# Kernel tuning notes

Measured on AMD Instinct MI355X. Metric: run time of the kernel, lower is better.

The kernel has to match this reference:

```python
import jax, jax.numpy as jnp
import numpy as np

N_NODES = 100000
N_EDGES = 1600000
D = 64


def setup_inputs() -> dict:
    key = jax.random.key(0)
    ks = jax.random.split(key, 8)
    x = jax.random.normal(ks[0], (N_NODES, D), dtype=jnp.float32)
    edge_index = jax.random.randint(ks[1], (2, N_EDGES), 0, N_NODES, dtype=jnp.int64)
    scale = 1.0 / np.sqrt(D)
    W1 = jax.random.normal(ks[2], (D, D), dtype=jnp.float32) * scale
    W2 = jax.random.normal(ks[3], (D, D), dtype=jnp.float32) * scale
    W3 = jax.random.normal(ks[4], (D, D), dtype=jnp.float32) * scale
    b1 = jnp.zeros((D,), dtype=jnp.float32)
    b2 = jnp.zeros((D,), dtype=jnp.float32)
    b3 = jnp.zeros((D,), dtype=jnp.float32)
    return {"x": x, "edge_index": edge_index, "W1": W1, "b1": b1,
            "W2": W2, "b2": b2, "W3": W3, "b3": b3}


def reference(x, edge_index, W1, b1, W2, b2, W3, b3):
    # 3-layer GCN (PyG GCNConv semantics): add self-loops, symmetric
    # degree normalization, linear transform, scatter-add aggregation.
    # Dropout is identity at inference.
    N = x.shape[0]
    loops = jnp.arange(N, dtype=edge_index.dtype)
    src = jnp.concatenate([edge_index[0], loops])  # [E+N]
    dst = jnp.concatenate([edge_index[1], loops])  # [E+N]
    # degree of each node (in-degree at dst, self-loops included)
    deg = jax.ops.segment_sum(jnp.ones(src.shape[0], dtype=x.dtype), dst,
                              num_segments=N)
    dis = jnp.where(deg > 0, jax.lax.rsqrt(jnp.maximum(deg, 1.0)), 0.0)
    norm = dis[src] * dis[dst]  # [E+N]

    def gcn_layer(h, W, b):
        h = h @ W                                   # [N, d_out]
        msg = norm[:, None] * h[src]                # gather + scale, [E+N, d_out]
        agg = jax.ops.segment_sum(msg, dst, num_segments=N)  # scatter-add
        return agg + b

    h = jax.nn.relu(gcn_layer(x, W1, b1))
    h = jax.nn.relu(gcn_layer(h, W2, b2))
    return gcn_layer(h, W3, b3)
```

## Files before the change

### kernel.cpp

```cpp
#include <hip/hip_runtime.h>

#define NN 100000
#define NE 1600000

typedef __attribute__((ext_vector_type(16))) int i32x16;

#define NBKT 391
#define NBLK 256
#define EPB  (NE / NBLK)
#define PTH  512
#define TOT  (NBKT * NBLK)
#define SB   ((TOT + 1023) / 1024)

__global__ __launch_bounds__(PTH) void k_pcount(const int* __restrict__ dst,
                                                int* __restrict__ pcount) {
  __shared__ int lcnt[NBKT];
  int t = threadIdx.x, b = blockIdx.x;
  for (int i = t; i < NBKT; i += PTH) lcnt[i] = 0;
  __syncthreads();
  int base = b * EPB;
  for (int i = t; i < EPB; i += PTH)
    atomicAdd(&lcnt[dst[base + i] >> 8], 1);
  __syncthreads();
  for (int i = t; i < NBKT; i += PTH)
    pcount[i * NBLK + b] = lcnt[i];
}

__global__ __launch_bounds__(256) void k_pscan1(int* __restrict__ pcount,
                                                int* __restrict__ bsum) {
  __shared__ int sh[256];
  int t = threadIdx.x, b = blockIdx.x;
  int base = b * 1024 + t * 4;
  int v0 = (base + 0 < TOT) ? pcount[base + 0] : 0;
  int v1 = (base + 1 < TOT) ? pcount[base + 1] : 0;
  int v2 = (base + 2 < TOT) ? pcount[base + 2] : 0;
  int v3 = (base + 3 < TOT) ? pcount[base + 3] : 0;
  int s = v0 + v1 + v2 + v3;
  sh[t] = s;
  __syncthreads();
  for (int off = 1; off < 256; off <<= 1) {
    int x = (t >= off) ? sh[t - off] : 0;
    __syncthreads();
    sh[t] += x;
    __syncthreads();
  }
  int ex = sh[t] - s;
  if (t == 255) bsum[b] = sh[255];
  if (base + 0 < TOT) pcount[base + 0] = ex; ex += v0;
  if (base + 1 < TOT) pcount[base + 1] = ex; ex += v1;
  if (base + 2 < TOT) pcount[base + 2] = ex; ex += v2;
  if (base + 3 < TOT) pcount[base + 3] = ex;
}

__global__ __launch_bounds__(128) void k_pscan2(int* __restrict__ bsum) {
  __shared__ int sh[128];
  int t = threadIdx.x;
  int v = (t < SB) ? bsum[t] : 0;
  sh[t] = v;
  __syncthreads();
  for (int off = 1; off < 128; off <<= 1) {
    int x = (t >= off) ? sh[t - off] : 0;
    __syncthreads();
    sh[t] += x;
    __syncthreads();
  }
  if (t < SB) bsum[t] = sh[t] - v;
}

__global__ __launch_bounds__(256) void k_pscan3(int* __restrict__ pcount,
                                                const int* __restrict__ bsum) {
  int t = threadIdx.x, b = blockIdx.x;
  int add = bsum[b];
  int base = b * 1024 + t * 4;
  #pragma unroll
  for (int k = 0; k < 4; ++k)
    if (base + k < TOT) pcount[base + k] += add;
}

__global__ __launch_bounds__(PTH) void k_pscatter(const int* __restrict__ src,
                                                  const int* __restrict__ dst,
                                                  const int* __restrict__ pcount,
                                                  int* __restrict__ staged) {
  __shared__ int lpos[NBKT];
  int t = threadIdx.x, b = blockIdx.x;
  for (int i = t; i < NBKT; i += PTH) lpos[i] = pcount[i * NBLK + b];
  __syncthreads();
  int base = b * EPB;
  for (int i = t; i < EPB; i += PTH) {
    int s = src[base + i], d = dst[base + i];
    int pos = atomicAdd(&lpos[d >> 8], 1);
    staged[pos] = s | ((d & 255) << 17);
  }
}

__global__ __launch_bounds__(PTH) void k_bucket(const int* __restrict__ staged,
                                                const int* __restrict__ pcount,
                                                int* __restrict__ rowptr,
                                                float* __restrict__ dis,
                                                int* __restrict__ col) {
  __shared__ int lcnt[256];
  __shared__ int lscan[PTH];
  __shared__ int lpos[256];
  int t = threadIdx.x, bkt = blockIdx.x;
  int sbeg = pcount[bkt * NBLK];
  int send = (bkt == NBKT - 1) ? NE : pcount[(bkt + 1) * NBLK];

  if (t < 256) lcnt[t] = 0;
  __syncthreads();
  for (int i = sbeg + t; i < send; i += PTH)
    atomicAdd(&lcnt[(unsigned)staged[i] >> 17], 1);
  __syncthreads();

  int v = (t < 256) ? lcnt[t] : 0;
  lscan[t] = v;
  __syncthreads();
  for (int off = 1; off < PTH; off <<= 1) {
    int x = (t >= off) ? lscan[t - off] : 0;
    __syncthreads();
    lscan[t] += x;
    __syncthreads();
  }
  if (t < 256) {
    int gbase = sbeg + lscan[t] - v;
    int node = bkt * 256 + t;
    if (node < NN) {
      rowptr[node] = gbase;
      dis[node] = rsqrtf((float)(v + 1));
    }
    lpos[t] = gbase;
    if (bkt == NBKT - 1 && t == 0) rowptr[NN] = NE;
  }
  __syncthreads();

  for (int i = sbeg + t; i < send; i += PTH) {
    int e = staged[i];
    col[atomicAdd(&lpos[(unsigned)e >> 17], 1)] = e & 0x1FFFF;
  }
}

__device__ __forceinline__ unsigned bf16rne(float x) {
  unsigned u = __float_as_uint(x);
  return (u + 0x7fffu + ((u >> 16) & 1u)) >> 16;
}

__global__ __launch_bounds__(256) void k_xform(const float* __restrict__ h,
                                               const float* __restrict__ W,
                                               const float* __restrict__ dis,
                                               unsigned short* __restrict__ ts) {
  __shared__ float hT[64][132];
  __shared__ float Wl[64][68];
  const int tid = threadIdx.x;
  const int R0 = blockIdx.x * 128;

  {
    const float4* W4 = (const float4*)W;
    #pragma unroll
    for (int j = 0; j < 4; ++j) {
      int idx = tid + 256 * j;
      float4 v = W4[idx];
      int k = idx >> 4;
      int c = (idx & 15) * 4;
      Wl[k][c + 0] = v.x; Wl[k][c + 1] = v.y;
      Wl[k][c + 2] = v.z; Wl[k][c + 3] = v.w;
    }
  }
  {
    #pragma unroll
    for (int j = 0; j < 8; ++j) {
      int idx = tid + 256 * j;
      int r = idx >> 4;
      int k = (idx & 15) * 4;
      int rg = R0 + r; if (rg > NN - 1) rg = NN - 1;
      float4 v = *(const float4*)(h + (size_t)rg * 64 + k);
      hT[k + 0][r] = v.x; hT[k + 1][r] = v.y;
      hT[k + 2][r] = v.z; hT[k + 3][r] = v.w;
    }
  }
  __syncthreads();

  const int tx = tid & 7;
  const int ty = tid >> 3;
  float acc[4][8];
  #pragma unroll
  for (int i = 0; i < 4; ++i)
    #pragma unroll
    for (int j = 0; j < 8; ++j) acc[i][j] = 0.f;

  #pragma unroll 4
  for (int k = 0; k < 64; ++k) {
    float4 hv = *(const float4*)&hT[k][ty * 4];
    float4 w0 = *(const float4*)&Wl[k][tx * 8];
    float4 w1 = *(const float4*)&Wl[k][tx * 8 + 4];
    float hh[4] = {hv.x, hv.y, hv.z, hv.w};
    float wc[8] = {w0.x, w0.y, w0.z, w0.w, w1.x, w1.y, w1.z, w1.w};
    #pragma unroll
    for (int i = 0; i < 4; ++i)
      #pragma unroll
      for (int j = 0; j < 8; ++j)
        acc[i][j] = fmaf(hh[i], wc[j], acc[i][j]);
  }

  #pragma unroll
  for (int i = 0; i < 4; ++i) {
    int r = R0 + ty * 4 + i;
    if (r < NN) {
      float dr = dis[r];
      uint4 pk;
      pk.x = bf16rne(acc[i][0] * dr) | (bf16rne(acc[i][1] * dr) << 16);
      pk.y = bf16rne(acc[i][2] * dr) | (bf16rne(acc[i][3] * dr) << 16);
      pk.z = bf16rne(acc[i][4] * dr) | (bf16rne(acc[i][5] * dr) << 16);
      pk.w = bf16rne(acc[i][6] * dr) | (bf16rne(acc[i][7] * dr) << 16);
      *(uint4*)(ts + (size_t)r * 64 + tx * 8) = pk;
    }
  }
}

__global__ __launch_bounds__(256) void k_fuse(
    const unsigned short* __restrict__ ts, const int* __restrict__ rowptr,
    const int* __restrict__ col, const float* __restrict__ dis,
    const float* __restrict__ bias, const float* __restrict__ Wn,
    unsigned short* __restrict__ tnext)
{
  __shared__ float Wl[64][68];
  __shared__ float hh[32][68];
  const int tid  = threadIdx.x;
  const int lane = tid & 63;
  const int slot = lane >> 4;
  const int fq   = lane & 15;
  const int R0   = blockIdx.x * 32;
  const int wloc = tid >> 6;
  const int wid  = __builtin_amdgcn_readfirstlane(
                     (int)(blockIdx.x * 4 + wloc));
  const int n0   = wid * 8;

  {
    const float4* W4 = (const float4*)Wn;
    #pragma unroll
    for (int j = 0; j < 4; ++j) {
      int idx = tid + 256 * j;
      float4 v = W4[idx];
      int k = idx >> 4;
      int c = (idx & 15) * 4;
      Wl[k][c + 0] = v.x; Wl[k][c + 1] = v.y;
      Wl[k][c + 2] = v.z; Wl[k][c + 3] = v.w;
    }
  }

  const float4 bv = *(const float4*)(bias + fq * 4);
  const float m_self = (slot == 0) ? 1.f : 0.f;

  i32x16 rp;
  asm volatile("s_load_dwordx16 %0, %1, 0x0\n\ts_waitcnt lgkmcnt(0)"
               : "=s"(rp) : "s"(rowptr + n0));

  float a[8][4];
  #pragma unroll
  for (int i = 0; i < 8; ++i) {
    const uint2 sv = *(const uint2*)(ts + (size_t)(n0 + i) * 64 + fq * 4);
    a[i][0] = m_self * __uint_as_float(sv.x << 16);
    a[i][1] = m_self * __uint_as_float(sv.x & 0xffff0000u);
    a[i][2] = m_self * __uint_as_float(sv.y << 16);
    a[i][3] = m_self * __uint_as_float(sv.y & 0xffff0000u);
  }

  #pragma unroll
  for (int i = 0; i < 8; ++i) {
    const int r0 = rp[i], r1 = rp[i + 1];
    #pragma unroll
    for (int s = 0; s < 4; ++s) {
      int e = r0 + s * 4 + slot;
      int c = col[e];
      bool valid = e < r1;
      c = valid ? c : 0;
      float m = valid ? 1.f : 0.f;
      const uint2 gv = *(const uint2*)(ts + (size_t)c * 64 + fq * 4);
      a[i][0] = fmaf(m, __uint_as_float(gv.x << 16),         a[i][0]);
      a[i][1] = fmaf(m, __uint_as_float(gv.x & 0xffff0000u), a[i][1]);
      a[i][2] = fmaf(m, __uint_as_float(gv.y << 16),         a[i][2]);
      a[i][3] = fmaf(m, __uint_as_float(gv.y & 0xffff0000u), a[i][3]);
    }
  }

  #pragma unroll
  for (int i = 0; i < 8; ++i) {
    const int r1 = rp[i + 1];
    #pragma unroll 1
    for (int e0 = rp[i] + 16; e0 < r1; e0 += 8) {
      #pragma unroll
      for (int s = 0; s < 2; ++s) {
        int e = e0 + s * 4 + slot;
        int c = col[e];
        bool valid = e < r1;
        c = valid ? c : 0;
        float m = valid ? 1.f : 0.f;
        const uint2 gv = *(const uint2*)(ts + (size_t)c * 64 + fq * 4);
        a[i][0] = fmaf(m, __uint_as_float(gv.x << 16),         a[i][0]);
        a[i][1] = fmaf(m, __uint_as_float(gv.x & 0xffff0000u), a[i][1]);
        a[i][2] = fmaf(m, __uint_as_float(gv.y << 16),         a[i][2]);
        a[i][3] = fmaf(m, __uint_as_float(gv.y & 0xffff0000u), a[i][3]);
      }
    }
  }

  #pragma unroll
  for (int i = 0; i < 8; ++i) {
    const int node = n0 + i;
    const float dn = dis[node];
    float s0 = a[i][0], s1 = a[i][1], s2 = a[i][2], s3 = a[i][3];
    s0 += __shfl_xor(s0, 16); s1 += __shfl_xor(s1, 16);
    s2 += __shfl_xor(s2, 16); s3 += __shfl_xor(s3, 16);
    s0 += __shfl_xor(s0, 32); s1 += __shfl_xor(s1, 32);
    s2 += __shfl_xor(s2, 32); s3 += __shfl_xor(s3, 32);
    float4 o;
    o.x = fmaxf(fmaf(dn, s0, bv.x), 0.f);
    o.y = fmaxf(fmaf(dn, s1, bv.y), 0.f);
    o.z = fmaxf(fmaf(dn, s2, bv.z), 0.f);
    o.w = fmaxf(fmaf(dn, s3, bv.w), 0.f);
    if (lane < 16)
      *(float4*)&hh[wloc * 8 + i][fq * 4] = o;
  }
  __syncthreads();

  const int tx = tid & 7;
  const int ty = tid >> 3;
  float acc[8];
  #pragma unroll
  for (int j = 0; j < 8; ++j) acc[j] = 0.f;
  #pragma unroll 4
  for (int k = 0; k < 64; ++k) {
    float hkv = hh[ty][k];
    float4 w0 = *(const float4*)&Wl[k][tx * 8];
    float4 w1 = *(const float4*)&Wl[k][tx * 8 + 4];
    acc[0] = fmaf(hkv, w0.x, acc[0]); acc[1] = fmaf(hkv, w0.y, acc[1]);
    acc[2] = fmaf(hkv, w0.z, acc[2]); acc[3] = fmaf(hkv, w0.w, acc[3]);
    acc[4] = fmaf(hkv, w1.x, acc[4]); acc[5] = fmaf(hkv, w1.y, acc[5]);
    acc[6] = fmaf(hkv, w1.z, acc[6]); acc[7] = fmaf(hkv, w1.w, acc[7]);
  }
  {
    int r = R0 + ty;
    float dr = dis[r];
    uint4 pk;
    pk.x = bf16rne(acc[0] * dr) | (bf16rne(acc[1] * dr) << 16);
    pk.y = bf16rne(acc[2] * dr) | (bf16rne(acc[3] * dr) << 16);
    pk.z = bf16rne(acc[4] * dr) | (bf16rne(acc[5] * dr) << 16);
    pk.w = bf16rne(acc[6] * dr) | (bf16rne(acc[7] * dr) << 16);
    *(uint4*)(tnext + (size_t)r * 64 + tx * 8) = pk;
  }
}

__global__ __launch_bounds__(256) void k_agg(
    const unsigned short* __restrict__ ts, const int* __restrict__ rowptr,
    const int* __restrict__ col, const float* __restrict__ dis,
    const float* __restrict__ bias, float* __restrict__ out)
{
  const int lane = threadIdx.x & 63;
  const int slot = lane >> 4;
  const int fq   = lane & 15;
  const int wid  = __builtin_amdgcn_readfirstlane(
                     (int)((blockIdx.x * blockDim.x + threadIdx.x) >> 6));
  const int n0   = wid * 8;
  if (n0 >= NN) return;

  const float4 bv = *(const float4*)(bias + fq * 4);
  const float m_self = (slot == 0) ? 1.f : 0.f;

  i32x16 rp;
  asm volatile("s_load_dwordx16 %0, %1, 0x0\n\ts_waitcnt lgkmcnt(0)"
               : "=s"(rp) : "s"(rowptr + n0));

  float a[8][4];
  #pragma unroll
  for (int i = 0; i < 8; ++i) {
    const uint2 sv = *(const uint2*)(ts + (size_t)(n0 + i) * 64 + fq * 4);
    a[i][0] = m_self * __uint_as_float(sv.x << 16);
    a[i][1] = m_self * __uint_as_float(sv.x & 0xffff0000u);
    a[i][2] = m_self * __uint_as_float(sv.y << 16);
    a[i][3] = m_self * __uint_as_float(sv.y & 0xffff0000u);
  }

  #pragma unroll
  for (int i = 0; i < 8; ++i) {
    const int r0 = rp[i], r1 = rp[i + 1];
    #pragma unroll
    for (int s = 0; s < 4; ++s) {
      int e = r0 + s * 4 + slot;
      int c = col[e];
      bool valid = e < r1;
      c = valid ? c : 0;
      float m = valid ? 1.f : 0.f;
      const uint2 gv = *(const uint2*)(ts + (size_t)c * 64 + fq * 4);
      a[i][0] = fmaf(m, __uint_as_float(gv.x << 16),         a[i][0]);
      a[i][1] = fmaf(m, __uint_as_float(gv.x & 0xffff0000u), a[i][1]);
      a[i][2] = fmaf(m, __uint_as_float(gv.y << 16),         a[i][2]);
      a[i][3] = fmaf(m, __uint_as_float(gv.y & 0xffff0000u), a[i][3]);
    }
  }

  #pragma unroll
  for (int i = 0; i < 8; ++i) {
    const int r1 = rp[i + 1];
    #pragma unroll 1
    for (int e0 = rp[i] + 16; e0 < r1; e0 += 8) {
      #pragma unroll
      for (int s = 0; s < 2; ++s) {
        int e = e0 + s * 4 + slot;
        int c = col[e];
        bool valid = e < r1;
        c = valid ? c : 0;
        float m = valid ? 1.f : 0.f;
        const uint2 gv = *(const uint2*)(ts + (size_t)c * 64 + fq * 4);
        a[i][0] = fmaf(m, __uint_as_float(gv.x << 16),         a[i][0]);
        a[i][1] = fmaf(m, __uint_as_float(gv.x & 0xffff0000u), a[i][1]);
        a[i][2] = fmaf(m, __uint_as_float(gv.y << 16),         a[i][2]);
        a[i][3] = fmaf(m, __uint_as_float(gv.y & 0xffff0000u), a[i][3]);
      }
    }
  }

  #pragma unroll
  for (int i = 0; i < 8; ++i) {
    const int node = n0 + i;
    const float dn = dis[node];
    float s0 = a[i][0], s1 = a[i][1], s2 = a[i][2], s3 = a[i][3];
    s0 += __shfl_xor(s0, 16); s1 += __shfl_xor(s1, 16);
    s2 += __shfl_xor(s2, 16); s3 += __shfl_xor(s3, 16);
    s0 += __shfl_xor(s0, 32); s1 += __shfl_xor(s1, 32);
    s2 += __shfl_xor(s2, 32); s3 += __shfl_xor(s3, 32);
    float4 o;
    o.x = fmaf(dn, s0, bv.x); o.y = fmaf(dn, s1, bv.y);
    o.z = fmaf(dn, s2, bv.z); o.w = fmaf(dn, s3, bv.w);
    if (lane < 16)
      *(float4*)(out + (size_t)node * 64 + fq * 4) = o;
  }
}

extern "C" void kernel_launch(void* const* d_in, const int* in_sizes, int n_in,
                              void* d_out, int out_size, void* d_ws, size_t ws_size,
                              hipStream_t stream) {
  const float* x  = (const float*)d_in[0];
  const int*   ei = (const int*)d_in[1];
  const float* W1 = (const float*)d_in[2];
  const float* b1 = (const float*)d_in[3];
  const float* W2 = (const float*)d_in[4];
  const float* b2 = (const float*)d_in[5];
  const float* W3 = (const float*)d_in[6];
  const float* b3 = (const float*)d_in[7];
  float* out = (float*)d_out;

  const int* src = ei;
  const int* dst = ei + NE;

  char* ws = (char*)d_ws;
  size_t off = 0;
  auto alloc = [&](size_t bytes) {
    void* p = ws + off;
    off = (off + bytes + 255) & ~(size_t)255;
    return p;
  };
  int*   pcount = (int*)alloc((size_t)TOT * 4);
  int*   bsum   = (int*)alloc((size_t)SB * 4);
  int*   rowptr = (int*)alloc((size_t)(NN + 1 + 16) * 4);
  float* dis    = (float*)alloc((size_t)NN * 4);
  int*   staged = (int*)alloc((size_t)NE * 4);
  int*   col    = (int*)alloc((size_t)(NE + 64) * 4);
  unsigned short* tb1 =
      (unsigned short*)alloc((size_t)NN * 64 * 2);
  unsigned short* tb2 =
      (unsigned short*)alloc((size_t)NN * 64 * 2);
  (void)ws_size; (void)in_sizes; (void)n_in; (void)out_size;

  k_pcount  <<<NBLK, PTH, 0, stream>>>(dst, pcount);
  k_pscan1  <<<SB, 256, 0, stream>>>(pcount, bsum);
  k_pscan2  <<<1, 128, 0, stream>>>(bsum);
  k_pscan3  <<<SB, 256, 0, stream>>>(pcount, bsum);
  k_pscatter<<<NBLK, PTH, 0, stream>>>(src, dst, pcount, staged);
  k_bucket  <<<NBKT, PTH, 0, stream>>>(staged, pcount, rowptr, dis, col);

  const int XF_BLOCKS = (NN + 127) / 128;
  const int FB        = NN / 32;

  k_xform<<<XF_BLOCKS, 256, 0, stream>>>(x, W1, dis, tb1);
  k_fuse <<<FB, 256, 0, stream>>>(tb1, rowptr, col, dis, b1, W2, tb2);
  k_fuse <<<FB, 256, 0, stream>>>(tb2, rowptr, col, dis, b2, W3, tb1);
  k_agg  <<<FB, 256, 0, stream>>>(tb1, rowptr, col, dis, b3, out);
}
```

Before: 183.8 us.

## Process 64 nodes per k_fuse block with 2-row register-blocked transform

```diff
diff --git a/kernel.cpp b/kernel.cpp
--- a/kernel.cpp
+++ b/kernel.cpp
@@ -222,16 +222,14 @@
     unsigned short* __restrict__ tnext)
 {
   __shared__ float Wl[64][68];
-  __shared__ float hh[32][68];
+  __shared__ float hh[64][68];
   const int tid  = threadIdx.x;
   const int lane = tid & 63;
   const int slot = lane >> 4;
   const int fq   = lane & 15;
-  const int R0   = blockIdx.x * 32;
+  const int R0   = blockIdx.x * 64;
   const int wloc = tid >> 6;
-  const int wid  = __builtin_amdgcn_readfirstlane(
-                     (int)(blockIdx.x * 4 + wloc));
-  const int n0   = wid * 8;
+  const int wbase = __builtin_amdgcn_readfirstlane(R0 + wloc * 16);
 
   {
     const float4* W4 = (const float4*)Wn;
@@ -245,106 +243,130 @@
       Wl[k][c + 2] = v.z; Wl[k][c + 3] = v.w;
     }
   }
+  __syncthreads();
 
   const float4 bv = *(const float4*)(bias + fq * 4);
   const float m_self = (slot == 0) ? 1.f : 0.f;
 
-  i32x16 rp;
-  asm volatile("s_load_dwordx16 %0, %1, 0x0\n\ts_waitcnt lgkmcnt(0)"
-               : "=s"(rp) : "s"(rowptr + n0));
-
-  float a[8][4];
-  #pragma unroll
-  for (int i = 0; i < 8; ++i) {
-    const uint2 sv = *(const uint2*)(ts + (size_t)(n0 + i) * 64 + fq * 4);
-    a[i][0] = m_self * __uint_as_float(sv.x << 16);
-    a[i][1] = m_self * __uint_as_float(sv.x & 0xffff0000u);
-    a[i][2] = m_self * __uint_as_float(sv.y << 16);
-    a[i][3] = m_self * __uint_as_float(sv.y & 0xffff0000u);
-  }
-
-  #pragma unroll
-  for (int i = 0; i < 8; ++i) {
-    const int r0 = rp[i], r1 = rp[i + 1];
-    #pragma unroll
-    for (int s = 0; s < 4; ++s) {
-      int e = r0 + s * 4 + slot;
-      int c = col[e];
-      bool valid = e < r1;
-      c = valid ? c : 0;
-      float m = valid ? 1.f : 0.f;
-      const uint2 gv = *(const uint2*)(ts + (size_t)c * 64 + fq * 4);
-      a[i][0] = fmaf(m, __uint_as_float(gv.x << 16),         a[i][0]);
-      a[i][1] = fmaf(m, __uint_as_float(gv.x & 0xffff0000u), a[i][1]);
-      a[i][2] = fmaf(m, __uint_as_float(gv.y << 16),         a[i][2]);
-      a[i][3] = fmaf(m, __uint_as_float(gv.y & 0xffff0000u), a[i][3]);
-    }
-  }
-
-  #pragma unroll
-  for (int i = 0; i < 8; ++i) {
-    const int r1 = rp[i + 1];
-    #pragma unroll 1
-    for (int e0 = rp[i] + 16; e0 < r1; e0 += 8) {
-      #pragma unroll
-      for (int s = 0; s < 2; ++s) {
-        int e = e0 + s * 4 + slot;
-        int c = col[e];
-        bool valid = e < r1;
-        c = valid ? c : 0;
-        float m = valid ? 1.f : 0.f;
-        const uint2 gv = *(const uint2*)(ts + (size_t)c * 64 + fq * 4);
-        a[i][0] = fmaf(m, __uint_as_float(gv.x << 16),         a[i][0]);
-        a[i][1] = fmaf(m, __uint_as_float(gv.x & 0xffff0000u), a[i][1]);
-        a[i][2] = fmaf(m, __uint_as_float(gv.y << 16),         a[i][2]);
-        a[i][3] = fmaf(m, __uint_as_float(gv.y & 0xffff0000u), a[i][3]);
+  #pragma unroll 2
+  for (int half = 0; half < 2; ++half) {
+    const int n0 = wbase + half * 8;
+    if (n0 < NN) {
+      i32x16 rp;
+      asm volatile("s_load_dwordx16 %0, %1, 0x0\n\ts_waitcnt lgkmcnt(0)"
+                   : "=s"(rp) : "s"(rowptr + n0));
+
+      float a[8][4];
+      #pragma unroll
+      for (int i = 0; i < 8; ++i) {
+        const uint2 sv = *(const uint2*)(ts + (size_t)(n0 + i) * 64 + fq * 4);
+        a[i][0] = m_self * __uint_as_float(sv.x << 16);
+        a[i][1] = m_self * __uint_as_float(sv.x & 0xffff0000u);
+        a[i][2] = m_self * __uint_as_float(sv.y << 16);
+        a[i][3] = m_self * __uint_as_float(sv.y & 0xffff0000u);
       }
-    }
-  }
-
-  #pragma unroll
-  for (int i = 0; i < 8; ++i) {
-    const int node = n0 + i;
-    const float dn = dis[node];
-    float s0 = a[i][0], s1 = a[i][1], s2 = a[i][2], s3 = a[i][3];
-    s0 += __shfl_xor(s0, 16); s1 += __shfl_xor(s1, 16);
-    s2 += __shfl_xor(s2, 16); s3 += __shfl_xor(s3, 16);
-    s0 += __shfl_xor(s0, 32); s1 += __shfl_xor(s1, 32);
-    s2 += __shfl_xor(s2, 32); s3 += __shfl_xor(s3, 32);
-    float4 o;
-    o.x = fmaxf(fmaf(dn, s0, bv.x), 0.f);
-    o.y = fmaxf(fmaf(dn, s1, bv.y), 0.f);
-    o.z = fmaxf(fmaf(dn, s2, bv.z), 0.f);
-    o.w = fmaxf(fmaf(dn, s3, bv.w), 0.f);
-    if (lane < 16)
-      *(float4*)&hh[wloc * 8 + i][fq * 4] = o;
-  }
-  __syncthreads();
-
-  const int tx = tid & 7;
-  const int ty = tid >> 3;
-  float acc[8];
-  #pragma unroll
-  for (int j = 0; j < 8; ++j) acc[j] = 0.f;
-  #pragma unroll 4
-  for (int k = 0; k < 64; ++k) {
-    float hkv = hh[ty][k];
-    float4 w0 = *(const float4*)&Wl[k][tx * 8];
-    float4 w1 = *(const float4*)&Wl[k][tx * 8 + 4];
-    acc[0] = fmaf(hkv, w0.x, acc[0]); acc[1] = fmaf(hkv, w0.y, acc[1]);
-    acc[2] = fmaf(hkv, w0.z, acc[2]); acc[3] = fmaf(hkv, w0.w, acc[3]);
-    acc[4] = fmaf(hkv, w1.x, acc[4]); acc[5] = fmaf(hkv, w1.y, acc[5]);
-    acc[6] = fmaf(hkv, w1.z, acc[6]); acc[7] = fmaf(hkv, w1.w, acc[7]);
-  }
-  {
-    int r = R0 + ty;
-    float dr = dis[r];
-    uint4 pk;
-    pk.x = bf16rne(acc[0] * dr) | (bf16rne(acc[1] * dr) << 16);
-    pk.y = bf16rne(acc[2] * dr) | (bf16rne(acc[3] * dr) << 16);
-    pk.z = bf16rne(acc[4] * dr) | (bf16rne(acc[5] * dr) << 16);
-    pk.w = bf16rne(acc[6] * dr) | (bf16rne(acc[7] * dr) << 16);
-    *(uint4*)(tnext + (size_t)r * 64 + tx * 8) = pk;
+
+      #pragma unroll
+      for (int i = 0; i < 8; ++i) {
+        const int r0 = rp[i], r1 = rp[i + 1];
+        #pragma unroll
+        for (int s = 0; s < 4; ++s) {
+          int e = r0 + s * 4 + slot;
+          int c = col[e];
+          bool valid = e < r1;
+          c = valid ? c : 0;
+          float m = valid ? 1.f : 0.f;
+          const uint2 gv = *(const uint2*)(ts + (size_t)c * 64 + fq * 4);
+          a[i][0] = fmaf(m, __uint_as_float(gv.x << 16),         a[i][0]);
+          a[i][1] = fmaf(m, __uint_as_float(gv.x & 0xffff0000u), a[i][1]);
+          a[i][2] = fmaf(m, __uint_as_float(gv.y << 16),         a[i][2]);
+          a[i][3] = fmaf(m, __uint_as_float(gv.y & 0xffff0000u), a[i][3]);
+        }
+      }
+
+      #pragma unroll
+      for (int i = 0; i < 8; ++i) {
+        const int r1 = rp[i + 1];
+        #pragma unroll 1
+        for (int e0 = rp[i] + 16; e0 < r1; e0 += 8) {
+          #pragma unroll
+          for (int s = 0; s < 2; ++s) {
+            int e = e0 + s * 4 + slot;
+            int c = col[e];
+            bool valid = e < r1;
+            c = valid ? c : 0;
+            float m = valid ? 1.f : 0.f;
+            const uint2 gv = *(const uint2*)(ts + (size_t)c * 64 + fq * 4);
+            a[i][0] = fmaf(m, __uint_as_float(gv.x << 16),         a[i][0]);
+            a[i][1] = fmaf(m, __uint_as_float(gv.x & 0xffff0000u), a[i][1]);
+            a[i][2] = fmaf(m, __uint_as_float(gv.y << 16),         a[i][2]);
+            a[i][3] = fmaf(m, __uint_as_float(gv.y & 0xffff0000u), a[i][3]);
+          }
+        }
+      }
+
+      #pragma unroll
+      for (int i = 0; i < 8; ++i) {
+        const int node = n0 + i;
+        const float dn = dis[node];
+        float s0 = a[i][0], s1 = a[i][1], s2 = a[i][2], s3 = a[i][3];
+        s0 += __shfl_xor(s0, 16); s1 += __shfl_xor(s1, 16);
+        s2 += __shfl_xor(s2, 16); s3 += __shfl_xor(s3, 16);
+        s0 += __shfl_xor(s0, 32); s1 += __shfl_xor(s1, 32);
+        s2 += __shfl_xor(s2, 32); s3 += __shfl_xor(s3, 32);
+        float4 o;
+        o.x = fmaxf(fmaf(dn, s0, bv.x), 0.f);
+        o.y = fmaxf(fmaf(dn, s1, bv.y), 0.f);
+        o.z = fmaxf(fmaf(dn, s2, bv.z), 0.f);
+        o.w = fmaxf(fmaf(dn, s3, bv.w), 0.f);
+        if (lane < 16)
+          *(float4*)&hh[wloc * 16 + half * 8 + i][fq * 4] = o;
+      }
+    }
+  }
+
+  const int cg = lane & 7;
+  const int lr = wloc * 16 + (lane >> 3) * 2;
+  float acc[2][8];
+  #pragma unroll
+  for (int i = 0; i < 2; ++i)
+    #pragma unroll
+    for (int j = 0; j < 8; ++j) acc[i][j] = 0.f;
+
+  #pragma unroll 2
+  for (int kk = 0; kk < 16; ++kk) {
+    float4 h0 = *(const float4*)&hh[lr][kk * 4];
+    float4 h1 = *(const float4*)&hh[lr + 1][kk * 4];
+    float h0a[4] = {h0.x, h0.y, h0.z, h0.w};
+    float h1a[4] = {h1.x, h1.y, h1.z, h1.w};
+    #pragma unroll
+    for (int j4 = 0; j4 < 4; ++j4) {
+      const int k = kk * 4 + j4;
+      float4 w0 = *(const float4*)&Wl[k][cg * 8];
+      float4 w1 = *(const float4*)&Wl[k][cg * 8 + 4];
+      float wc[8] = {w0.x, w0.y, w0.z, w0.w, w1.x, w1.y, w1.z, w1.w};
+      #pragma unroll
+      for (int j = 0; j < 8; ++j) {
+        acc[0][j] = fmaf(h0a[j4], wc[j], acc[0][j]);
+        acc[1][j] = fmaf(h1a[j4], wc[j], acc[1][j]);
+      }
+    }
+  }
+
+  #pragma unroll
+  for (int i = 0; i < 2; ++i) {
+    const int r = R0 + (lr - R0 % 64) + i;
+    const int rr = R0 + (wloc * 16 + (lane >> 3) * 2) + i;
+    if (rr < NN) {
+      float dr = dis[rr];
+      uint4 pk;
+      pk.x = bf16rne(acc[i][0] * dr) | (bf16rne(acc[i][1] * dr) << 16);
+      pk.y = bf16rne(acc[i][2] * dr) | (bf16rne(acc[i][3] * dr) << 16);
+      pk.z = bf16rne(acc[i][4] * dr) | (bf16rne(acc[i][5] * dr) << 16);
+      pk.w = bf16rne(acc[i][6] * dr) | (bf16rne(acc[i][7] * dr) << 16);
+      *(uint4*)(tnext + (size_t)rr * 64 + cg * 8) = pk;
+    }
+    (void)r;
   }
 }
 
@@ -477,10 +499,11 @@
   k_bucket  <<<NBKT, PTH, 0, stream>>>(staged, pcount, rowptr, dis, col);
 
   const int XF_BLOCKS = (NN + 127) / 128;
-  const int FB        = NN / 32;
+  const int FU_BLOCKS = (NN + 63) / 64;
+  const int AG_BLOCKS = NN / 32;
 
   k_xform<<<XF_BLOCKS, 256, 0, stream>>>(x, W1, dis, tb1);
-  k_fuse <<<FB, 256, 0, stream>>>(tb1, rowptr, col, dis, b1, W2, tb2);
-  k_fuse <<<FB, 256, 0, stream>>>(tb2, rowptr, col, dis, b2, W3, tb1);
-  k_agg  <<<FB, 256, 0, stream>>>(tb1, rowptr, col, dis, b3, out);
-}
+  k_fuse <<<FU_BLOCKS, 256, 0, stream>>>(tb1, rowptr, col, dis, b1, W2, tb2);
+  k_fuse <<<FU_BLOCKS, 256, 0, stream>>>(tb2, rowptr, col, dis, b2, W3, tb1);
+  k_agg  <<<AG_BLOCKS, 256, 0, stream>>>(tb1, rowptr, col, dis, b3, out);
+}
```

New measurement: 195.1 us. +6.1%, slower.
